# Optimization experiments

Measured on AMD Instinct MI355X. Metric: run time of the kernel, lower is better.

## Reference

```python
import jax, jax.numpy as jnp
import numpy as np

B, T, D = 4, 2048, 1024
E, K = 8, 2
H = int(D * 2.0)  # d_hidden


def setup_inputs() -> dict:
    key = jax.random.key(0)
    ks = jax.random.split(key, 7)
    x = jax.random.normal(ks[0], (B, T, D), dtype=jnp.float32)
    # router Linear(d_model, n_experts)
    router_w = jax.random.normal(ks[1], (D, E), dtype=jnp.float32) * (1.0 / np.sqrt(D))
    router_b = jnp.zeros((E,), dtype=jnp.float32)
    # expert weights, xavier_uniform-like scale
    lim1 = float(np.sqrt(6.0 / (D + H)))
    lim2 = float(np.sqrt(6.0 / (H + D)))
    w1 = jax.random.uniform(ks[2], (E, D, H), dtype=jnp.float32, minval=-lim1, maxval=lim1)
    b1 = jnp.zeros((E, H), dtype=jnp.float32)
    w2 = jax.random.uniform(ks[3], (E, H, D), dtype=jnp.float32, minval=-lim2, maxval=lim2)
    b2 = jnp.zeros((E, D), dtype=jnp.float32)
    return {"x": x, "router_w": router_w, "router_b": router_b,
            "w1": w1, "b1": b1, "w2": w2, "b2": b2}


def reference(x, router_w, router_b, w1, b1, w2, b2):
    Bs, Ts, d = x.shape
    N = Bs * Ts
    h = x.reshape(N, d)
    logits = h @ router_w + router_b                      # [N, E]
    probs = jax.nn.softmax(logits, axis=-1)
    weights, indices = jax.lax.top_k(probs, K)            # [N, K]
    weights = weights / (jnp.sum(weights, axis=-1, keepdims=True) + 1e-9)
    rows = jnp.arange(N)[:, None]
    # routing mask M and combine weights G (scatter over expert axis)
    M = jnp.zeros((N, E), dtype=bool).at[rows, indices].set(True)
    G = jnp.zeros((N, E), dtype=x.dtype).at[rows, indices].add(weights)
    # dense expert compute; tokens with G[:,e]==0 contribute nothing,
    # matching the masked gather/scatter loop exactly (dropout=0, eval mode)
    hidden = jax.nn.gelu(jnp.einsum('nd,edh->enh', h, w1) + b1[:, None, :],
                         approximate=False)               # [E, N, H]
    expert_out = jnp.einsum('enh,ehd->end', hidden, w2) + b2[:, None, :]  # [E, N, D]
    y = jnp.einsum('ne,end->nd', G, expert_out)           # combine
    y = y.reshape(Bs, Ts, d)
    # aux losses
    f_e = M.astype(jnp.float32).mean(axis=0)
    P_e = probs.mean(axis=0)
    lb_loss = -E * jnp.sum(f_e * P_e)
    z = jax.nn.logsumexp(logits, axis=-1)
    z_loss = jnp.mean(z ** 2)
    entropy = jnp.mean(-jnp.sum(probs * jnp.log(probs + 1e-10), axis=-1))
    return (y, lb_loss, z_loss, entropy, f_e, P_e)
```

## Files before the change

kernel.cpp:

```cpp
#include <hip/hip_runtime.h>
#include <hip/hip_bf16.h>

#define NTOK 8192
#define DM 1024
#define NE 8
#define DH 2048
#define CAP 18432

typedef __attribute__((ext_vector_type(8))) short short8;
typedef __attribute__((ext_vector_type(4))) float float4v;

#define ASYNC_COPY16(gsrc, ldst)                                                              \
    __builtin_amdgcn_global_load_lds((const __attribute__((address_space(1))) unsigned int*)(gsrc), \
                                     (__attribute__((address_space(3))) unsigned int*)(ldst), \
                                     16, 0, 0)

static __device__ __forceinline__ unsigned short f2bf(float f) {
    __hip_bfloat16 h = __float2bfloat16(f);
    return *reinterpret_cast<unsigned short*>(&h);
}

static __device__ __forceinline__ float fast_gelu(float v) {
    float x = v * 0.70710678118654752f;
    float ax = fabsf(x);
    float t = __frcp_rn(1.0f + 0.3275911f * ax);
    float poly = ((((1.061405429f * t - 1.453152027f) * t + 1.421413741f) * t
                   - 0.284496736f) * t + 0.254829592f) * t;
    float y = 1.0f - poly * __expf(-ax * ax);
    float erfv = copysignf(y, x);
    return 0.5f * v * (1.0f + erfv);
}


__global__ __launch_bounds__(256) void k_transpose(const float* __restrict__ src,
                                                   __hip_bfloat16* __restrict__ dst,
                                                   int R, int C) {
    __shared__ float t[64][65];
    size_t mat = (size_t)blockIdx.z * R * C;
    src += mat;
    dst += mat;
    int c0 = blockIdx.x * 64, r0 = blockIdx.y * 64;
    int tx = threadIdx.x & 63, ty = threadIdx.x >> 6;
#pragma unroll
    for (int i = 0; i < 16; i++) {
        int r = ty + i * 4;
        t[r][tx] = src[(size_t)(r0 + r) * C + c0 + tx];
    }
    __syncthreads();
    int rx = (threadIdx.x & 15) * 4;
    int cy = threadIdx.x >> 4;
#pragma unroll
    for (int i = 0; i < 4; i++) {
        int c = cy + i * 16;
        ushort4 v;
        v.x = f2bf(t[rx + 0][c]);
        v.y = f2bf(t[rx + 1][c]);
        v.z = f2bf(t[rx + 2][c]);
        v.w = f2bf(t[rx + 3][c]);
        *(ushort4*)((unsigned short*)dst + (size_t)(c0 + c) * R + r0 + rx) = v;
    }
}


__global__ __launch_bounds__(256) void k_router(const float* __restrict__ x,
                                                const float* __restrict__ rw,
                                                const float* __restrict__ rb,
                                                __hip_bfloat16* __restrict__ xb,
                                                int* __restrict__ topidx,
                                                float* __restrict__ topw,
                                                float* __restrict__ probs8,
                                                float* __restrict__ zent) {
    int lane = threadIdx.x & 63, wv = threadIdx.x >> 6;
    int n = blockIdx.x * 4 + wv;
    const float* xr = x + (size_t)n * DM;
    unsigned short* xbr = (unsigned short*)xb + (size_t)n * DM;
    float p[8] = {0.f, 0.f, 0.f, 0.f, 0.f, 0.f, 0.f, 0.f};
#pragma unroll
    for (int i = 0; i < 16; i++) {
        int d = lane + i * 64;
        float xv = xr[d];
        xbr[d] = f2bf(xv);
        const float4* w4 = (const float4*)(rw + (size_t)d * 8);
        float4 wa = w4[0], wb = w4[1];
        p[0] += xv * wa.x; p[1] += xv * wa.y; p[2] += xv * wa.z; p[3] += xv * wa.w;
        p[4] += xv * wb.x; p[5] += xv * wb.y; p[6] += xv * wb.z; p[7] += xv * wb.w;
    }
#pragma unroll
    for (int e = 0; e < 8; e++) {
#pragma unroll
        for (int off = 32; off > 0; off >>= 1) p[e] += __shfl_down(p[e], off);
    }
    if (lane == 0) {
        float logits[8], probs[8];
        float mx = -1e30f;
#pragma unroll
        for (int e = 0; e < 8; e++) {
            logits[e] = p[e] + rb[e];
            mx = fmaxf(mx, logits[e]);
        }
        float se = 0.f;
#pragma unroll
        for (int e = 0; e < 8; e++) {
            probs[e] = __expf(logits[e] - mx);
            se += probs[e];
        }
        float inv = 1.f / se;
        float z = mx + logf(se);
        float ent = 0.f;
#pragma unroll
        for (int e = 0; e < 8; e++) {
            probs[e] *= inv;
            ent -= probs[e] * logf(probs[e] + 1e-10f);
        }
        int i0 = 0;
#pragma unroll
        for (int e = 1; e < 8; e++)
            if (probs[e] > probs[i0]) i0 = e;
        int i1 = (i0 == 0) ? 1 : 0;
#pragma unroll
        for (int e = 0; e < 8; e++)
            if (e != i0 && e != i1 && probs[e] > probs[i1]) i1 = e;
        float w0 = probs[i0], w1v = probs[i1];
        float s = w0 + w1v + 1e-9f;
        topidx[2 * n] = i0;
        topidx[2 * n + 1] = i1;
        topw[2 * n] = w0 / s;
        topw[2 * n + 1] = w1v / s;
        float* pr = probs8 + (size_t)n * 8;
#pragma unroll
        for (int e = 0; e < 8; e++) pr[e] = probs[e];
        zent[2 * n] = z * z;
        zent[2 * n + 1] = ent;
    }
}


__global__ __launch_bounds__(256) void k_stats(const int* __restrict__ topidx,
                                               const float* __restrict__ probs8,
                                               const float* __restrict__ zent,
                                               float* __restrict__ fcnt,
                                               float* __restrict__ sump,
                                               float* __restrict__ szent) {
    int n = blockIdx.x * 256 + threadIdx.x;
    float v[18];
    int e0 = topidx[2 * n], e1 = topidx[2 * n + 1];
#pragma unroll
    for (int e = 0; e < 8; e++) v[e] = (float)((e == e0) + (e == e1));
    const float4* p4 = (const float4*)(probs8 + (size_t)n * 8);
    float4 pa = p4[0], pb = p4[1];
    v[8] = pa.x; v[9] = pa.y; v[10] = pa.z; v[11] = pa.w;
    v[12] = pb.x; v[13] = pb.y; v[14] = pb.z; v[15] = pb.w;
    v[16] = zent[2 * n];
    v[17] = zent[2 * n + 1];
#pragma unroll
    for (int i = 0; i < 18; i++)
#pragma unroll
        for (int off = 32; off > 0; off >>= 1) v[i] += __shfl_down(v[i], off);
    __shared__ float part[4][18];
    int lane = threadIdx.x & 63, wv = threadIdx.x >> 6;
    if (lane == 0)
#pragma unroll
        for (int i = 0; i < 18; i++) part[wv][i] = v[i];
    __syncthreads();
    if (threadIdx.x == 0) {
#pragma unroll
        for (int i = 0; i < 18; i++) {
            float s = part[0][i] + part[1][i] + part[2][i] + part[3][i];
            if (i < 8) atomicAdd(&fcnt[i], s);
            else if (i < 16) atomicAdd(&sump[i - 8], s);
            else atomicAdd(&szent[i - 16], s);
        }
    }
}


__global__ void k_scan(const float* __restrict__ fcnt, int* __restrict__ offs) {
    if (threadIdx.x == 0 && blockIdx.x == 0) {
        int o = 0;
        for (int e = 0; e < NE; e++) {
            offs[e] = o;
            int c = (int)(fcnt[e] + 0.5f);
            o += (c + 255) & ~255;
        }
        offs[NE] = o;
    }
}

__global__ __launch_bounds__(256) void k_scatter(const int* __restrict__ topidx,
                                                 const float* __restrict__ topw,
                                                 const int* __restrict__ offs,
                                                 int* __restrict__ cnt2,
                                                 int* __restrict__ rowtok,
                                                 float* __restrict__ roww) {
    __shared__ int lcnt[8], lbase[8];
    int tid = threadIdx.x;
    if (tid < 8) lcnt[tid] = 0;
    __syncthreads();
    int n = blockIdx.x * 256 + tid;
    int e0 = topidx[2 * n], e1 = topidx[2 * n + 1];
    int p0 = atomicAdd(&lcnt[e0], 1);
    int p1 = atomicAdd(&lcnt[e1], 1);
    __syncthreads();
    if (tid < 8) lbase[tid] = atomicAdd(&cnt2[tid], lcnt[tid]);
    __syncthreads();
    int r0 = offs[e0] + lbase[e0] + p0;
    int r1 = offs[e1] + lbase[e1] + p1;
    rowtok[r0] = n; roww[r0] = topw[2 * n];
    rowtok[r1] = n; roww[r1] = topw[2 * n + 1];
}


#define KT1 (DM / 32)

__global__ __launch_bounds__(512) void k_gemm1(const __hip_bfloat16* __restrict__ xb,
                                               const __hip_bfloat16* __restrict__ w1T,
                                               const float* __restrict__ b1,
                                               const int* __restrict__ rowtok,
                                               const int* __restrict__ offs,
                                               __hip_bfloat16* __restrict__ hid) {
    int bid = blockIdx.x;
    int ib = bid >> 3;
    int row0 = ((bid & 7) * 9 + (ib >> 4)) * 256;
    if (row0 >= offs[NE]) return;
    int h0 = (ib & 15) * 128;
    int e = 0;
    while (row0 >= offs[e + 1]) e++;
    int tid = threadIdx.x;

    __shared__ __align__(16) short lds[3][12288];
    __shared__ int tokoff[256];
    if (tid < 256) {
        int t = rowtok[row0 + tid];
        tokoff[tid] = (t < 0 ? 0 : t) * DM;
    }
    __syncthreads();

    int sr = tid >> 2, pc = tid & 3;
    int ch = pc ^ ((sr >> 1) & 3);
    const short* aS0 = (const short*)xb + tokoff[sr] + ch * 8;
    const short* aS1 = (const short*)xb + tokoff[128 + sr] + ch * 8;
    const short* bS  = (const short*)w1T + ((size_t)e * DH + h0 + sr) * DM + ch * 8;
    int ldo = sr * 32 + pc * 8;

    int lane = tid & 63, wv = tid >> 6;
    int wm = (wv >> 1) * 64, wn = (wv & 1) * 64;
    int quad = lane >> 4, l16 = lane & 15;
    int a_off[4], b_off[4];
#pragma unroll
    for (int mt = 0; mt < 4; mt++) {
        int r = wm + mt * 16 + l16;
        a_off[mt] = r * 32 + ((quad ^ ((r >> 1) & 3)) * 8);
    }
#pragma unroll
    for (int nt = 0; nt < 4; nt++) {
        int r = wn + nt * 16 + l16;
        b_off[nt] = 8192 + r * 32 + ((quad ^ ((r >> 1) & 3)) * 8);
    }
    float4v acc[4][4];
#pragma unroll
    for (int i = 0; i < 4; i++)
#pragma unroll
        for (int j = 0; j < 4; j++) {
            float4v z = {0.f, 0.f, 0.f, 0.f};
            acc[i][j] = z;
        }

    ASYNC_COPY16(aS0, &lds[0][ldo]);
    ASYNC_COPY16(aS1, &lds[0][4096 + ldo]);
    ASYNC_COPY16(bS,  &lds[0][8192 + ldo]);
    ASYNC_COPY16(aS0 + 32, &lds[1][ldo]);
    ASYNC_COPY16(aS1 + 32, &lds[1][4096 + ldo]);
    ASYNC_COPY16(bS + 32,  &lds[1][8192 + ldo]);
    asm volatile("s_waitcnt vmcnt(3)" ::: "memory");
    asm volatile("s_barrier" ::: "memory");

    int bi = 0;
#pragma unroll 1
    for (int t = 0; t < KT1; ++t) {
        const short* Ab = &lds[bi][0];
        int sbi = bi + 2; if (sbi >= 3) sbi -= 3;
        int k2 = (t + 2) * 32;
        short8 af[4], bf[4];
#pragma unroll
        for (int mt = 0; mt < 4; mt++) af[mt] = *(const short8*)(Ab + a_off[mt]);
#pragma unroll
        for (int nt = 0; nt < 4; nt++) bf[nt] = *(const short8*)(Ab + b_off[nt]);
        if (t + 2 < KT1) {
            ASYNC_COPY16(aS0 + k2, &lds[sbi][ldo]);
            ASYNC_COPY16(aS1 + k2, &lds[sbi][4096 + ldo]);
            ASYNC_COPY16(bS + k2,  &lds[sbi][8192 + ldo]);
        }
        __builtin_amdgcn_s_setprio(1);
#pragma unroll
        for (int mt = 0; mt < 4; mt++)
#pragma unroll
            for (int nt = 0; nt < 4; nt++)
                acc[mt][nt] = __builtin_amdgcn_mfma_f32_16x16x32_bf16(af[mt], bf[nt], acc[mt][nt], 0, 0, 0);
        __builtin_amdgcn_s_setprio(0);
        if (t + 2 < KT1) asm volatile("s_waitcnt vmcnt(3)" ::: "memory");
        else             asm volatile("s_waitcnt vmcnt(0)" ::: "memory");
        asm volatile("s_barrier" ::: "memory");
        bi++; if (bi == 3) bi = 0;
    }

    const float* b1e = b1 + (size_t)e * DH + h0;
#pragma unroll
    for (int mt = 0; mt < 4; mt++) {
#pragma unroll
        for (int nt = 0; nt < 4; nt++) {
            int rl = wm + mt * 16 + quad * 4;
            int cl = wn + nt * 16 + l16;
            float bias = b1e[cl];
#pragma unroll
            for (int r = 0; r < 4; r++) {
                float v = fast_gelu(acc[mt][nt][r] + bias);
                hid[(size_t)(row0 + rl + r) * DH + h0 + cl] = __float2bfloat16(v);
            }
        }
    }
}


#define KT2 (DH / 32)

__global__ __launch_bounds__(512) void k_gemm2(const __hip_bfloat16* __restrict__ hid,
                                               const __hip_bfloat16* __restrict__ w2T,
                                               const float* __restrict__ b2,
                                               const float* __restrict__ roww,
                                               const int* __restrict__ rowtok,
                                               const int* __restrict__ offs,
                                               float* __restrict__ y) {
    int bid = blockIdx.x;
    int ib = bid >> 3;
    int row0 = ((bid & 7) * 9 + (ib >> 3)) * 256;
    if (row0 >= offs[NE]) return;
    int d0 = (ib & 7) * 128;
    int e = 0;
    while (row0 >= offs[e + 1]) e++;
    int tid = threadIdx.x;

    __shared__ __align__(16) short lds[3][12288];
    __shared__ int tok_s[256];
    __shared__ float rw_s[256];
    if (tid < 256) {
        tok_s[tid] = rowtok[row0 + tid];
        rw_s[tid] = roww[row0 + tid];
    }
    __syncthreads();

    int sr = tid >> 2, pc = tid & 3;
    int ch = pc ^ ((sr >> 1) & 3);
    const short* aS0 = (const short*)hid + (size_t)(row0 + sr) * DH + ch * 8;
    const short* aS1 = (const short*)hid + (size_t)(row0 + 128 + sr) * DH + ch * 8;
    const short* bS  = (const short*)w2T + ((size_t)e * DM + d0 + sr) * DH + ch * 8;
    int ldo = sr * 32 + pc * 8;

    int lane = tid & 63, wv = tid >> 6;
    int wm = (wv >> 1) * 64, wn = (wv & 1) * 64;
    int quad = lane >> 4, l16 = lane & 15;
    int a_off[4], b_off[4];
#pragma unroll
    for (int mt = 0; mt < 4; mt++) {
        int r = wm + mt * 16 + l16;
        a_off[mt] = r * 32 + ((quad ^ ((r >> 1) & 3)) * 8);
    }
#pragma unroll
    for (int nt = 0; nt < 4; nt++) {
        int r = wn + nt * 16 + l16;
        b_off[nt] = 8192 + r * 32 + ((quad ^ ((r >> 1) & 3)) * 8);
    }
    float4v acc[4][4];
#pragma unroll
    for (int i = 0; i < 4; i++)
#pragma unroll
        for (int j = 0; j < 4; j++) {
            float4v z = {0.f, 0.f, 0.f, 0.f};
            acc[i][j] = z;
        }

    ASYNC_COPY16(aS0, &lds[0][ldo]);
    ASYNC_COPY16(aS1, &lds[0][4096 + ldo]);
    ASYNC_COPY16(bS,  &lds[0][8192 + ldo]);
    ASYNC_COPY16(aS0 + 32, &lds[1][ldo]);
    ASYNC_COPY16(aS1 + 32, &lds[1][4096 + ldo]);
    ASYNC_COPY16(bS + 32,  &lds[1][8192 + ldo]);
    asm volatile("s_waitcnt vmcnt(3)" ::: "memory");
    asm volatile("s_barrier" ::: "memory");

    int bi = 0;
#pragma unroll 1
    for (int t = 0; t < KT2; ++t) {
        const short* Ab = &lds[bi][0];
        int sbi = bi + 2; if (sbi >= 3) sbi -= 3;
        int k2 = (t + 2) * 32;
        short8 af[4], bf[4];
#pragma unroll
        for (int mt = 0; mt < 4; mt++) af[mt] = *(const short8*)(Ab + a_off[mt]);
#pragma unroll
        for (int nt = 0; nt < 4; nt++) bf[nt] = *(const short8*)(Ab + b_off[nt]);
        if (t + 2 < KT2) {
            ASYNC_COPY16(aS0 + k2, &lds[sbi][ldo]);
            ASYNC_COPY16(aS1 + k2, &lds[sbi][4096 + ldo]);
            ASYNC_COPY16(bS + k2,  &lds[sbi][8192 + ldo]);
        }
        __builtin_amdgcn_s_setprio(1);
#pragma unroll
        for (int mt = 0; mt < 4; mt++)
#pragma unroll
            for (int nt = 0; nt < 4; nt++)
                acc[mt][nt] = __builtin_amdgcn_mfma_f32_16x16x32_bf16(af[mt], bf[nt], acc[mt][nt], 0, 0, 0);
        __builtin_amdgcn_s_setprio(0);
        if (t + 2 < KT2) asm volatile("s_waitcnt vmcnt(3)" ::: "memory");
        else             asm volatile("s_waitcnt vmcnt(0)" ::: "memory");
        asm volatile("s_barrier" ::: "memory");
        bi++; if (bi == 3) bi = 0;
    }

    const float* b2e = b2 + (size_t)e * DM + d0;
#pragma unroll
    for (int mt = 0; mt < 4; mt++) {
#pragma unroll
        for (int nt = 0; nt < 4; nt++) {
            int rl = wm + mt * 16 + quad * 4;
            int cl = wn + nt * 16 + l16;
            float bias = b2e[cl];
#pragma unroll
            for (int r = 0; r < 4; r++) {
                int lr = rl + r;
                int tk = tok_s[lr];
                if (tk >= 0) {
                    float v = (acc[mt][nt][r] + bias) * rw_s[lr];
                    atomicAdd(&y[(size_t)tk * DM + d0 + cl], v);
                }
            }
        }
    }
}


__global__ void k_finalize(const float* __restrict__ fcnt, const float* __restrict__ sump,
                           const float* __restrict__ szent, float* __restrict__ out) {
    if (threadIdx.x == 0 && blockIdx.x == 0) {
        const float invN = 1.0f / (float)NTOK;
        float lb = 0.f;
        float f[NE], P[NE];
        for (int e = 0; e < NE; e++) {
            f[e] = fcnt[e] * invN;
            P[e] = sump[e] * invN;
            lb += f[e] * P[e];
        }
        size_t base = (size_t)NTOK * DM;
        out[base + 0] = -(float)NE * lb;
        out[base + 1] = szent[0] * invN;
        out[base + 2] = szent[1] * invN;
        for (int e = 0; e < NE; e++) out[base + 3 + e] = f[e];
        for (int e = 0; e < NE; e++) out[base + 11 + e] = P[e];
    }
}


extern "C" void kernel_launch(void* const* d_in, const int* in_sizes, int n_in,
                              void* d_out, int out_size, void* d_ws, size_t ws_size,
                              hipStream_t stream) {
    const float* x  = (const float*)d_in[0];
    const float* rw = (const float*)d_in[1];
    const float* rb = (const float*)d_in[2];
    const float* w1 = (const float*)d_in[3];
    const float* b1 = (const float*)d_in[4];
    const float* w2 = (const float*)d_in[5];
    const float* b2 = (const float*)d_in[6];
    float* out = (float*)d_out;

    char* ws = (char*)d_ws;
    size_t o = 0;
    auto alloc = [&](size_t bytes) {
        size_t r = o;
        o = (o + bytes + 255) & ~(size_t)255;
        return r;
    };
    __hip_bfloat16* w1T = (__hip_bfloat16*)(ws + alloc((size_t)NE * DM * DH * 2));
    __hip_bfloat16* w2T = (__hip_bfloat16*)(ws + alloc((size_t)NE * DM * DH * 2));
    __hip_bfloat16* xb  = (__hip_bfloat16*)(ws + alloc((size_t)NTOK * DM * 2));
    __hip_bfloat16* hid = (__hip_bfloat16*)(ws + alloc((size_t)CAP * DH * 2));
    int* rowtok = (int*)(ws + alloc(CAP * 4));
    size_t zstart = o;
    float* roww  = (float*)(ws + alloc(CAP * 4));
    float* fcnt  = (float*)(ws + alloc(64));
    int* cnt2    = (int*)(ws + alloc(64));
    int* offs    = (int*)(ws + alloc(64));
    float* sump  = (float*)(ws + alloc(64));
    float* szent = (float*)(ws + alloc(64));
    size_t zend = o;
    int* topidx = (int*)(ws + alloc((size_t)NTOK * 2 * 4));
    float* topw = (float*)(ws + alloc((size_t)NTOK * 2 * 4));
    float* probs8 = (float*)(ws + alloc((size_t)NTOK * 8 * 4));
    float* zent   = (float*)(ws + alloc((size_t)NTOK * 2 * 4));

    hipMemsetAsync(rowtok, 0xFF, (size_t)CAP * 4, stream);
    hipMemsetAsync(ws + zstart, 0, zend - zstart, stream);
    hipMemsetAsync(out, 0, (size_t)NTOK * DM * 4, stream);

    k_transpose<<<dim3(DH / 64, DM / 64, NE), 256, 0, stream>>>(w1, w1T, DM, DH);
    k_transpose<<<dim3(DM / 64, DH / 64, NE), 256, 0, stream>>>(w2, w2T, DH, DM);
    k_router<<<NTOK / 4, 256, 0, stream>>>(x, rw, rb, xb, topidx, topw, probs8, zent);
    k_stats<<<NTOK / 256, 256, 0, stream>>>(topidx, probs8, zent, fcnt, sump, szent);
    k_scan<<<1, 1, 0, stream>>>(fcnt, offs);
    k_scatter<<<NTOK / 256, 256, 0, stream>>>(topidx, topw, offs, cnt2, rowtok, roww);
    k_gemm1<<<1152, 512, 0, stream>>>(xb, w1T, b1, rowtok, offs, hid);
    k_gemm2<<<576, 512, 0, stream>>>(hid, w2T, b2, roww, rowtok, offs, out);
    k_finalize<<<1, 1, 0, stream>>>(fcnt, sump, szent, out);
}
```

Measured before the change: 496.1 us.

## Replace atomic scatter-add with per-slot output buffer and combine kernel; double-buffer GEMMs

GEMM2 now writes each expert row's weighted output to a dense per-slot buffer, and a new combine kernel sums each token's two slots into y. This removes the fp32 atomicAdd scatter and the memset of the output. Both GEMMs also drop from three to two LDS stages, which frees shared memory so the launch bound can target more resident blocks. The cost is an extra 75MB buffer written and read back, plus a shallower prefetch pipeline that waits on every load each iteration.

Result: slower. 1.670 ms (+236.6%).

```diff
diff --git a/kernel.cpp b/kernel.cpp
--- a/kernel.cpp
+++ b/kernel.cpp
@@ -191,7 +191,8 @@
                                                  const int* __restrict__ offs,
                                                  int* __restrict__ cnt2,
                                                  int* __restrict__ rowtok,
-                                                 float* __restrict__ roww) {
+                                                 float* __restrict__ roww,
+                                                 int* __restrict__ slot) {
     __shared__ int lcnt[8], lbase[8];
     int tid = threadIdx.x;
     if (tid < 8) lcnt[tid] = 0;
@@ -205,19 +206,19 @@
     __syncthreads();
     int r0 = offs[e0] + lbase[e0] + p0;
     int r1 = offs[e1] + lbase[e1] + p1;
-    rowtok[r0] = n; roww[r0] = topw[2 * n];
-    rowtok[r1] = n; roww[r1] = topw[2 * n + 1];
+    rowtok[r0] = n; roww[r0] = topw[2 * n];     slot[2 * n] = r0;
+    rowtok[r1] = n; roww[r1] = topw[2 * n + 1]; slot[2 * n + 1] = r1;
 }
 
 
 #define KT1 (DM / 32)
 
-__global__ __launch_bounds__(512) void k_gemm1(const __hip_bfloat16* __restrict__ xb,
-                                               const __hip_bfloat16* __restrict__ w1T,
-                                               const float* __restrict__ b1,
-                                               const int* __restrict__ rowtok,
-                                               const int* __restrict__ offs,
-                                               __hip_bfloat16* __restrict__ hid) {
+__global__ __launch_bounds__(512, 6) void k_gemm1(const __hip_bfloat16* __restrict__ xb,
+                                                  const __hip_bfloat16* __restrict__ w1T,
+                                                  const float* __restrict__ b1,
+                                                  const int* __restrict__ rowtok,
+                                                  const int* __restrict__ offs,
+                                                  __hip_bfloat16* __restrict__ hid) {
     int bid = blockIdx.x;
     int ib = bid >> 3;
     int row0 = ((bid & 7) * 9 + (ib >> 4)) * 256;
@@ -227,7 +228,7 @@
     while (row0 >= offs[e + 1]) e++;
     int tid = threadIdx.x;
 
-    __shared__ __align__(16) short lds[3][12288];
+    __shared__ __align__(16) short lds[2][12288];
     __shared__ int tokoff[256];
     if (tid < 256) {
         int t = rowtok[row0 + tid];
@@ -268,28 +269,24 @@
     ASYNC_COPY16(aS0, &lds[0][ldo]);
     ASYNC_COPY16(aS1, &lds[0][4096 + ldo]);
     ASYNC_COPY16(bS,  &lds[0][8192 + ldo]);
-    ASYNC_COPY16(aS0 + 32, &lds[1][ldo]);
-    ASYNC_COPY16(aS1 + 32, &lds[1][4096 + ldo]);
-    ASYNC_COPY16(bS + 32,  &lds[1][8192 + ldo]);
-    asm volatile("s_waitcnt vmcnt(3)" ::: "memory");
+    asm volatile("s_waitcnt vmcnt(0)" ::: "memory");
     asm volatile("s_barrier" ::: "memory");
 
-    int bi = 0;
+    int buf = 0;
 #pragma unroll 1
     for (int t = 0; t < KT1; ++t) {
-        const short* Ab = &lds[bi][0];
-        int sbi = bi + 2; if (sbi >= 3) sbi -= 3;
-        int k2 = (t + 2) * 32;
+        const short* Ab = &lds[buf][0];
+        int k1 = (t + 1) * 32;
+        if (t + 1 < KT1) {
+            ASYNC_COPY16(aS0 + k1, &lds[buf ^ 1][ldo]);
+            ASYNC_COPY16(aS1 + k1, &lds[buf ^ 1][4096 + ldo]);
+            ASYNC_COPY16(bS + k1,  &lds[buf ^ 1][8192 + ldo]);
+        }
         short8 af[4], bf[4];
 #pragma unroll
         for (int mt = 0; mt < 4; mt++) af[mt] = *(const short8*)(Ab + a_off[mt]);
 #pragma unroll
         for (int nt = 0; nt < 4; nt++) bf[nt] = *(const short8*)(Ab + b_off[nt]);
-        if (t + 2 < KT1) {
-            ASYNC_COPY16(aS0 + k2, &lds[sbi][ldo]);
-            ASYNC_COPY16(aS1 + k2, &lds[sbi][4096 + ldo]);
-            ASYNC_COPY16(bS + k2,  &lds[sbi][8192 + ldo]);
-        }
         __builtin_amdgcn_s_setprio(1);
 #pragma unroll
         for (int mt = 0; mt < 4; mt++)
@@ -297,10 +294,9 @@
             for (int nt = 0; nt < 4; nt++)
                 acc[mt][nt] = __builtin_amdgcn_mfma_f32_16x16x32_bf16(af[mt], bf[nt], acc[mt][nt], 0, 0, 0);
         __builtin_amdgcn_s_setprio(0);
-        if (t + 2 < KT1) asm volatile("s_waitcnt vmcnt(3)" ::: "memory");
-        else             asm volatile("s_waitcnt vmcnt(0)" ::: "memory");
+        asm volatile("s_waitcnt vmcnt(0)" ::: "memory");
         asm volatile("s_barrier" ::: "memory");
-        bi++; if (bi == 3) bi = 0;
+        buf ^= 1;
     }
 
     const float* b1e = b1 + (size_t)e * DH + h0;
@@ -323,13 +319,12 @@
 
 #define KT2 (DH / 32)
 
-__global__ __launch_bounds__(512) void k_gemm2(const __hip_bfloat16* __restrict__ hid,
-                                               const __hip_bfloat16* __restrict__ w2T,
-                                               const float* __restrict__ b2,
-                                               const float* __restrict__ roww,
-                                               const int* __restrict__ rowtok,
-                                               const int* __restrict__ offs,
-                                               float* __restrict__ y) {
+__global__ __launch_bounds__(512, 6) void k_gemm2(const __hip_bfloat16* __restrict__ hid,
+                                                  const __hip_bfloat16* __restrict__ w2T,
+                                                  const float* __restrict__ b2,
+                                                  const float* __restrict__ roww,
+                                                  const int* __restrict__ offs,
+                                                  float* __restrict__ outb) {
     int bid = blockIdx.x;
     int ib = bid >> 3;
     int row0 = ((bid & 7) * 9 + (ib >> 3)) * 256;
@@ -339,14 +334,7 @@
     while (row0 >= offs[e + 1]) e++;
     int tid = threadIdx.x;
 
-    __shared__ __align__(16) short lds[3][12288];
-    __shared__ int tok_s[256];
-    __shared__ float rw_s[256];
-    if (tid < 256) {
-        tok_s[tid] = rowtok[row0 + tid];
-        rw_s[tid] = roww[row0 + tid];
-    }
-    __syncthreads();
+    __shared__ __align__(16) short lds[2][12288];
 
     int sr = tid >> 2, pc = tid & 3;
     int ch = pc ^ ((sr >> 1) & 3);
@@ -381,28 +369,24 @@
     ASYNC_COPY16(aS0, &lds[0][ldo]);
     ASYNC_COPY16(aS1, &lds[0][4096 + ldo]);
     ASYNC_COPY16(bS,  &lds[0][8192 + ldo]);
-    ASYNC_COPY16(aS0 + 32, &lds[1][ldo]);
-    ASYNC_COPY16(aS1 + 32, &lds[1][4096 + ldo]);
-    ASYNC_COPY16(bS + 32,  &lds[1][8192 + ldo]);
-    asm volatile("s_waitcnt vmcnt(3)" ::: "memory");
+    asm volatile("s_waitcnt vmcnt(0)" ::: "memory");
     asm volatile("s_barrier" ::: "memory");
 
-    int bi = 0;
+    int buf = 0;
 #pragma unroll 1
     for (int t = 0; t < KT2; ++t) {
-        const short* Ab = &lds[bi][0];
-        int sbi = bi + 2; if (sbi >= 3) sbi -= 3;
-        int k2 = (t + 2) * 32;
+        const short* Ab = &lds[buf][0];
+        int k1 = (t + 1) * 32;
+        if (t + 1 < KT2) {
+            ASYNC_COPY16(aS0 + k1, &lds[buf ^ 1][ldo]);
+            ASYNC_COPY16(aS1 + k1, &lds[buf ^ 1][4096 + ldo]);
+            ASYNC_COPY16(bS + k1,  &lds[buf ^ 1][8192 + ldo]);
+        }
         short8 af[4], bf[4];
 #pragma unroll
         for (int mt = 0; mt < 4; mt++) af[mt] = *(const short8*)(Ab + a_off[mt]);
 #pragma unroll
         for (int nt = 0; nt < 4; nt++) bf[nt] = *(const short8*)(Ab + b_off[nt]);
-        if (t + 2 < KT2) {
-            ASYNC_COPY16(aS0 + k2, &lds[sbi][ldo]);
-            ASYNC_COPY16(aS1 + k2, &lds[sbi][4096 + ldo]);
-            ASYNC_COPY16(bS + k2,  &lds[sbi][8192 + ldo]);
-        }
         __builtin_amdgcn_s_setprio(1);
 #pragma unroll
         for (int mt = 0; mt < 4; mt++)
@@ -410,10 +394,9 @@
             for (int nt = 0; nt < 4; nt++)
                 acc[mt][nt] = __builtin_amdgcn_mfma_f32_16x16x32_bf16(af[mt], bf[nt], acc[mt][nt], 0, 0, 0);
         __builtin_amdgcn_s_setprio(0);
-        if (t + 2 < KT2) asm volatile("s_waitcnt vmcnt(3)" ::: "memory");
-        else             asm volatile("s_waitcnt vmcnt(0)" ::: "memory");
+        asm volatile("s_waitcnt vmcnt(0)" ::: "memory");
         asm volatile("s_barrier" ::: "memory");
-        bi++; if (bi == 3) bi = 0;
+        buf ^= 1;
     }
 
     const float* b2e = b2 + (size_t)e * DM + d0;
@@ -426,17 +409,30 @@
             float bias = b2e[cl];
 #pragma unroll
             for (int r = 0; r < 4; r++) {
-                int lr = rl + r;
-                int tk = tok_s[lr];
-                if (tk >= 0) {
-                    float v = (acc[mt][nt][r] + bias) * rw_s[lr];
-                    atomicAdd(&y[(size_t)tk * DM + d0 + cl], v);
-                }
+                int grow = row0 + rl + r;
+                float v = (acc[mt][nt][r] + bias) * roww[grow];
+                outb[(size_t)grow * DM + d0 + cl] = v;
             }
         }
     }
 }
 
+
+__global__ __launch_bounds__(256) void k_combine(const float* __restrict__ outb,
+                                                 const int* __restrict__ slot,
+                                                 float* __restrict__ y) {
+    int n = blockIdx.x;
+    int r0 = slot[2 * n], r1 = slot[2 * n + 1];
+    const float4* p0 = (const float4*)(outb + (size_t)r0 * DM);
+    const float4* p1 = (const float4*)(outb + (size_t)r1 * DM);
+    float4 a = p0[threadIdx.x], b = p1[threadIdx.x];
+    float4 c;
+    c.x = a.x + b.x;
+    c.y = a.y + b.y;
+    c.z = a.z + b.z;
+    c.w = a.w + b.w;
+    ((float4*)(y + (size_t)n * DM))[threadIdx.x] = c;
+}
 
 __global__ void k_finalize(const float* __restrict__ fcnt, const float* __restrict__ sump,
                            const float* __restrict__ szent, float* __restrict__ out) {
@@ -482,6 +478,7 @@
     __hip_bfloat16* w2T = (__hip_bfloat16*)(ws + alloc((size_t)NE * DM * DH * 2));
     __hip_bfloat16* xb  = (__hip_bfloat16*)(ws + alloc((size_t)NTOK * DM * 2));
     __hip_bfloat16* hid = (__hip_bfloat16*)(ws + alloc((size_t)CAP * DH * 2));
+    float* outb = (float*)(ws + alloc((size_t)CAP * DM * 4));
     int* rowtok = (int*)(ws + alloc(CAP * 4));
     size_t zstart = o;
     float* roww  = (float*)(ws + alloc(CAP * 4));
@@ -493,20 +490,21 @@
     size_t zend = o;
     int* topidx = (int*)(ws + alloc((size_t)NTOK * 2 * 4));
     float* topw = (float*)(ws + alloc((size_t)NTOK * 2 * 4));
+    int* slot   = (int*)(ws + alloc((size_t)NTOK * 2 * 4));
     float* probs8 = (float*)(ws + alloc((size_t)NTOK * 8 * 4));
     float* zent   = (float*)(ws + alloc((size_t)NTOK * 2 * 4));
 
     hipMemsetAsync(rowtok, 0xFF, (size_t)CAP * 4, stream);
     hipMemsetAsync(ws + zstart, 0, zend - zstart, stream);
-    hipMemsetAsync(out, 0, (size_t)NTOK * DM * 4, stream);
 
     k_transpose<<<dim3(DH / 64, DM / 64, NE), 256, 0, stream>>>(w1, w1T, DM, DH);
     k_transpose<<<dim3(DM / 64, DH / 64, NE), 256, 0, stream>>>(w2, w2T, DH, DM);
     k_router<<<NTOK / 4, 256, 0, stream>>>(x, rw, rb, xb, topidx, topw, probs8, zent);
     k_stats<<<NTOK / 256, 256, 0, stream>>>(topidx, probs8, zent, fcnt, sump, szent);
     k_scan<<<1, 1, 0, stream>>>(fcnt, offs);
-    k_scatter<<<NTOK / 256, 256, 0, stream>>>(topidx, topw, offs, cnt2, rowtok, roww);
+    k_scatter<<<NTOK / 256, 256, 0, stream>>>(topidx, topw, offs, cnt2, rowtok, roww, slot);
     k_gemm1<<<1152, 512, 0, stream>>>(xb, w1T, b1, rowtok, offs, hid);
-    k_gemm2<<<576, 512, 0, stream>>>(hid, w2T, b2, roww, rowtok, offs, out);
+    k_gemm2<<<576, 512, 0, stream>>>(hid, w2T, b2, roww, offs, outb);
+    k_combine<<<NTOK, 256, 0, stream>>>(outb, slot, out);
     k_finalize<<<1, 1, 0, stream>>>(fcnt, sump, szent, out);
 }
```

## Fuse routing stats/scan/scatter into one kernel; replace atomic combine with gather pass

Applied to the files above, without the earlier changes.

Replaces the stats, scan, scatter and finalize kernels plus three memsets with a single-block routing kernel. It uses wave ballots to assign rows deterministically and computes the aux losses in the same pass. GEMM2 now writes weighted per-row outputs to a buffer instead of doing atomicAdd into y, and a new combine kernel sums each token's two rows. It also adds an extra barrier and sched_barriers in both GEMM main loops. The cost is an extra 75MB fp32 buffer round trip, and the single-block routing kernel is serial over 8192 tokens.

After: 536.5 us. +8.1%, slower.

```diff
diff --git a/kernel.cpp b/kernel.cpp
--- a/kernel.cpp
+++ b/kernel.cpp
@@ -135,78 +135,94 @@
 }
 
 
-__global__ __launch_bounds__(256) void k_stats(const int* __restrict__ topidx,
-                                               const float* __restrict__ probs8,
-                                               const float* __restrict__ zent,
-                                               float* __restrict__ fcnt,
-                                               float* __restrict__ sump,
-                                               float* __restrict__ szent) {
-    int n = blockIdx.x * 256 + threadIdx.x;
-    float v[18];
-    int e0 = topidx[2 * n], e1 = topidx[2 * n + 1];
-#pragma unroll
-    for (int e = 0; e < 8; e++) v[e] = (float)((e == e0) + (e == e1));
-    const float4* p4 = (const float4*)(probs8 + (size_t)n * 8);
-    float4 pa = p4[0], pb = p4[1];
-    v[8] = pa.x; v[9] = pa.y; v[10] = pa.z; v[11] = pa.w;
-    v[12] = pb.x; v[13] = pb.y; v[14] = pb.z; v[15] = pb.w;
-    v[16] = zent[2 * n];
-    v[17] = zent[2 * n + 1];
-#pragma unroll
-    for (int i = 0; i < 18; i++)
-#pragma unroll
-        for (int off = 32; off > 0; off >>= 1) v[i] += __shfl_down(v[i], off);
-    __shared__ float part[4][18];
-    int lane = threadIdx.x & 63, wv = threadIdx.x >> 6;
+__global__ __launch_bounds__(512) void k_route_aux(const int* __restrict__ topidx,
+                                                   const float* __restrict__ topw,
+                                                   const float* __restrict__ probs8,
+                                                   const float* __restrict__ zent,
+                                                   int* __restrict__ rowtok,
+                                                   float* __restrict__ roww,
+                                                   int* __restrict__ slot,
+                                                   int* __restrict__ offs,
+                                                   float* __restrict__ out) {
+    int tid = threadIdx.x, lane = tid & 63, wv = tid >> 6;
+    __shared__ int cnt_s[8];
+    __shared__ int offs_s[9];
+    __shared__ float red[8][10];
+    unsigned long long ltmask = ((unsigned long long)1 << lane) - 1ull;
+
+    int cnt = 0;
+    for (int i = lane; i < NTOK; i += 64) {
+        int2 v = ((const int2*)topidx)[i];
+        unsigned long long m0 = __ballot(v.x == wv);
+        unsigned long long m1 = __ballot(v.y == wv);
+        cnt += __popcll(m0) + __popcll(m1);
+    }
+    if (lane == 0) cnt_s[wv] = cnt;
+    __syncthreads();
+    if (tid == 0) {
+        int o = 0;
+        for (int e = 0; e < NE; e++) { offs_s[e] = o; o += (cnt_s[e] + 255) & ~255; }
+        offs_s[NE] = o;
+        for (int e = 0; e <= NE; e++) offs[e] = offs_s[e];
+    }
+    __syncthreads();
+    int base = offs_s[wv], pos = 0;
+    for (int i = lane; i < NTOK; i += 64) {
+        int2 v = ((const int2*)topidx)[i];
+        float2 w = ((const float2*)topw)[i];
+        unsigned long long m0 = __ballot(v.x == wv);
+        if (v.x == wv) {
+            int r = base + pos + __popcll(m0 & ltmask);
+            rowtok[r] = i; roww[r] = w.x; slot[2 * i] = r;
+        }
+        pos += __popcll(m0);
+        unsigned long long m1 = __ballot(v.y == wv);
+        if (v.y == wv) {
+            int r = base + pos + __popcll(m1 & ltmask);
+            rowtok[r] = i; roww[r] = w.y; slot[2 * i + 1] = r;
+        }
+        pos += __popcll(m1);
+    }
+    for (int r = base + cnt + lane; r < offs_s[wv + 1]; r += 64) {
+        rowtok[r] = -1; roww[r] = 0.f;
+    }
+    float s[10];
+#pragma unroll
+    for (int k = 0; k < 10; k++) s[k] = 0.f;
+    for (int i = tid; i < NTOK; i += 512) {
+        const float4* p4 = (const float4*)(probs8 + (size_t)i * 8);
+        float4 pa = p4[0], pb = p4[1];
+        s[0] += pa.x; s[1] += pa.y; s[2] += pa.z; s[3] += pa.w;
+        s[4] += pb.x; s[5] += pb.y; s[6] += pb.z; s[7] += pb.w;
+        float2 ze = ((const float2*)zent)[i];
+        s[8] += ze.x; s[9] += ze.y;
+    }
+#pragma unroll
+    for (int k = 0; k < 10; k++)
+#pragma unroll
+        for (int off = 32; off > 0; off >>= 1) s[k] += __shfl_down(s[k], off);
     if (lane == 0)
 #pragma unroll
-        for (int i = 0; i < 18; i++) part[wv][i] = v[i];
+        for (int k = 0; k < 10; k++) red[wv][k] = s[k];
     __syncthreads();
-    if (threadIdx.x == 0) {
-#pragma unroll
-        for (int i = 0; i < 18; i++) {
-            float s = part[0][i] + part[1][i] + part[2][i] + part[3][i];
-            if (i < 8) atomicAdd(&fcnt[i], s);
-            else if (i < 16) atomicAdd(&sump[i - 8], s);
-            else atomicAdd(&szent[i - 16], s);
-        }
-    }
-}
-
-
-__global__ void k_scan(const float* __restrict__ fcnt, int* __restrict__ offs) {
-    if (threadIdx.x == 0 && blockIdx.x == 0) {
-        int o = 0;
+    if (tid == 0) {
+        const float invN = 1.0f / (float)NTOK;
+        float lb = 0.f;
+        size_t b = (size_t)NTOK * DM;
         for (int e = 0; e < NE; e++) {
-            offs[e] = o;
-            int c = (int)(fcnt[e] + 0.5f);
-            o += (c + 255) & ~255;
-        }
-        offs[NE] = o;
-    }
-}
-
-__global__ __launch_bounds__(256) void k_scatter(const int* __restrict__ topidx,
-                                                 const float* __restrict__ topw,
-                                                 const int* __restrict__ offs,
-                                                 int* __restrict__ cnt2,
-                                                 int* __restrict__ rowtok,
-                                                 float* __restrict__ roww) {
-    __shared__ int lcnt[8], lbase[8];
-    int tid = threadIdx.x;
-    if (tid < 8) lcnt[tid] = 0;
-    __syncthreads();
-    int n = blockIdx.x * 256 + tid;
-    int e0 = topidx[2 * n], e1 = topidx[2 * n + 1];
-    int p0 = atomicAdd(&lcnt[e0], 1);
-    int p1 = atomicAdd(&lcnt[e1], 1);
-    __syncthreads();
-    if (tid < 8) lbase[tid] = atomicAdd(&cnt2[tid], lcnt[tid]);
-    __syncthreads();
-    int r0 = offs[e0] + lbase[e0] + p0;
-    int r1 = offs[e1] + lbase[e1] + p1;
-    rowtok[r0] = n; roww[r0] = topw[2 * n];
-    rowtok[r1] = n; roww[r1] = topw[2 * n + 1];
+            float sP = 0.f;
+            for (int w8 = 0; w8 < 8; w8++) sP += red[w8][e];
+            float fe = cnt_s[e] * invN, Pe = sP * invN;
+            lb += fe * Pe;
+            out[b + 3 + e] = fe;
+            out[b + 11 + e] = Pe;
+        }
+        float z2 = 0.f, en = 0.f;
+        for (int w8 = 0; w8 < 8; w8++) { z2 += red[w8][8]; en += red[w8][9]; }
+        out[b + 0] = -(float)NE * lb;
+        out[b + 1] = z2 * invN;
+        out[b + 2] = en * invN;
+    }
 }
 
 
@@ -290,6 +306,8 @@
             ASYNC_COPY16(aS1 + k2, &lds[sbi][4096 + ldo]);
             ASYNC_COPY16(bS + k2,  &lds[sbi][8192 + ldo]);
         }
+        asm volatile("s_barrier" ::: "memory");
+        __builtin_amdgcn_sched_barrier(0);
         __builtin_amdgcn_s_setprio(1);
 #pragma unroll
         for (int mt = 0; mt < 4; mt++)
@@ -297,6 +315,7 @@
             for (int nt = 0; nt < 4; nt++)
                 acc[mt][nt] = __builtin_amdgcn_mfma_f32_16x16x32_bf16(af[mt], bf[nt], acc[mt][nt], 0, 0, 0);
         __builtin_amdgcn_s_setprio(0);
+        __builtin_amdgcn_sched_barrier(0);
         if (t + 2 < KT1) asm volatile("s_waitcnt vmcnt(3)" ::: "memory");
         else             asm volatile("s_waitcnt vmcnt(0)" ::: "memory");
         asm volatile("s_barrier" ::: "memory");
@@ -327,9 +346,8 @@
                                                const __hip_bfloat16* __restrict__ w2T,
                                                const float* __restrict__ b2,
                                                const float* __restrict__ roww,
-                                               const int* __restrict__ rowtok,
                                                const int* __restrict__ offs,
-                                               float* __restrict__ y) {
+                                               float* __restrict__ outb) {
     int bid = blockIdx.x;
     int ib = bid >> 3;
     int row0 = ((bid & 7) * 9 + (ib >> 3)) * 256;
@@ -340,13 +358,6 @@
     int tid = threadIdx.x;
 
     __shared__ __align__(16) short lds[3][12288];
-    __shared__ int tok_s[256];
-    __shared__ float rw_s[256];
-    if (tid < 256) {
-        tok_s[tid] = rowtok[row0 + tid];
-        rw_s[tid] = roww[row0 + tid];
-    }
-    __syncthreads();
 
     int sr = tid >> 2, pc = tid & 3;
     int ch = pc ^ ((sr >> 1) & 3);
@@ -403,6 +414,8 @@
             ASYNC_COPY16(aS1 + k2, &lds[sbi][4096 + ldo]);
             ASYNC_COPY16(bS + k2,  &lds[sbi][8192 + ldo]);
         }
+        asm volatile("s_barrier" ::: "memory");
+        __builtin_amdgcn_sched_barrier(0);
         __builtin_amdgcn_s_setprio(1);
 #pragma unroll
         for (int mt = 0; mt < 4; mt++)
@@ -410,6 +423,7 @@
             for (int nt = 0; nt < 4; nt++)
                 acc[mt][nt] = __builtin_amdgcn_mfma_f32_16x16x32_bf16(af[mt], bf[nt], acc[mt][nt], 0, 0, 0);
         __builtin_amdgcn_s_setprio(0);
+        __builtin_amdgcn_sched_barrier(0);
         if (t + 2 < KT2) asm volatile("s_waitcnt vmcnt(3)" ::: "memory");
         else             asm volatile("s_waitcnt vmcnt(0)" ::: "memory");
         asm volatile("s_barrier" ::: "memory");
@@ -426,36 +440,29 @@
             float bias = b2e[cl];
 #pragma unroll
             for (int r = 0; r < 4; r++) {
-                int lr = rl + r;
-                int tk = tok_s[lr];
-                if (tk >= 0) {
-                    float v = (acc[mt][nt][r] + bias) * rw_s[lr];
-                    atomicAdd(&y[(size_t)tk * DM + d0 + cl], v);
-                }
+                int grow = row0 + rl + r;
+                float v = (acc[mt][nt][r] + bias) * roww[grow];
+                outb[(size_t)grow * DM + d0 + cl] = v;
             }
         }
     }
 }
 
 
-__global__ void k_finalize(const float* __restrict__ fcnt, const float* __restrict__ sump,
-                           const float* __restrict__ szent, float* __restrict__ out) {
-    if (threadIdx.x == 0 && blockIdx.x == 0) {
-        const float invN = 1.0f / (float)NTOK;
-        float lb = 0.f;
-        float f[NE], P[NE];
-        for (int e = 0; e < NE; e++) {
-            f[e] = fcnt[e] * invN;
-            P[e] = sump[e] * invN;
-            lb += f[e] * P[e];
-        }
-        size_t base = (size_t)NTOK * DM;
-        out[base + 0] = -(float)NE * lb;
-        out[base + 1] = szent[0] * invN;
-        out[base + 2] = szent[1] * invN;
-        for (int e = 0; e < NE; e++) out[base + 3 + e] = f[e];
-        for (int e = 0; e < NE; e++) out[base + 11 + e] = P[e];
-    }
+__global__ __launch_bounds__(256) void k_combine(const float* __restrict__ outb,
+                                                 const int* __restrict__ slot,
+                                                 float* __restrict__ y) {
+    int n = blockIdx.x;
+    int r0 = slot[2 * n], r1 = slot[2 * n + 1];
+    const float4* p0 = (const float4*)(outb + (size_t)r0 * DM);
+    const float4* p1 = (const float4*)(outb + (size_t)r1 * DM);
+    float4 a = p0[threadIdx.x], b = p1[threadIdx.x];
+    float4 c;
+    c.x = a.x + b.x;
+    c.y = a.y + b.y;
+    c.z = a.z + b.z;
+    c.w = a.w + b.w;
+    ((float4*)(y + (size_t)n * DM))[threadIdx.x] = c;
 }
 
 
@@ -482,31 +489,21 @@
     __hip_bfloat16* w2T = (__hip_bfloat16*)(ws + alloc((size_t)NE * DM * DH * 2));
     __hip_bfloat16* xb  = (__hip_bfloat16*)(ws + alloc((size_t)NTOK * DM * 2));
     __hip_bfloat16* hid = (__hip_bfloat16*)(ws + alloc((size_t)CAP * DH * 2));
+    float* outb = (float*)(ws + alloc((size_t)CAP * DM * 4));
     int* rowtok = (int*)(ws + alloc(CAP * 4));
-    size_t zstart = o;
-    float* roww  = (float*)(ws + alloc(CAP * 4));
-    float* fcnt  = (float*)(ws + alloc(64));
-    int* cnt2    = (int*)(ws + alloc(64));
-    int* offs    = (int*)(ws + alloc(64));
-    float* sump  = (float*)(ws + alloc(64));
-    float* szent = (float*)(ws + alloc(64));
-    size_t zend = o;
+    float* roww = (float*)(ws + alloc(CAP * 4));
+    int* offs   = (int*)(ws + alloc(64));
     int* topidx = (int*)(ws + alloc((size_t)NTOK * 2 * 4));
     float* topw = (float*)(ws + alloc((size_t)NTOK * 2 * 4));
+    int* slot   = (int*)(ws + alloc((size_t)NTOK * 2 * 4));
     float* probs8 = (float*)(ws + alloc((size_t)NTOK * 8 * 4));
     float* zent   = (float*)(ws + alloc((size_t)NTOK * 2 * 4));
-
-    hipMemsetAsync(rowtok, 0xFF, (size_t)CAP * 4, stream);
-    hipMemsetAsync(ws + zstart, 0, zend - zstart, stream);
-    hipMemsetAsync(out, 0, (size_t)NTOK * DM * 4, stream);
 
     k_transpose<<<dim3(DH / 64, DM / 64, NE), 256, 0, stream>>>(w1, w1T, DM, DH);
     k_transpose<<<dim3(DM / 64, DH / 64, NE), 256, 0, stream>>>(w2, w2T, DH, DM);
     k_router<<<NTOK / 4, 256, 0, stream>>>(x, rw, rb, xb, topidx, topw, probs8, zent);
-    k_stats<<<NTOK / 256, 256, 0, stream>>>(topidx, probs8, zent, fcnt, sump, szent);
-    k_scan<<<1, 1, 0, stream>>>(fcnt, offs);
-    k_scatter<<<NTOK / 256, 256, 0, stream>>>(topidx, topw, offs, cnt2, rowtok, roww);
+    k_route_aux<<<1, 512, 0, stream>>>(topidx, topw, probs8, zent, rowtok, roww, slot, offs, out);
     k_gemm1<<<1152, 512, 0, stream>>>(xb, w1T, b1, rowtok, offs, hid);
-    k_gemm2<<<576, 512, 0, stream>>>(hid, w2T, b2, roww, rowtok, offs, out);
-    k_finalize<<<1, 1, 0, stream>>>(fcnt, sump, szent, out);
-}
+    k_gemm2<<<576, 512, 0, stream>>>(hid, w2T, b2, roww, offs, outb);
+    k_combine<<<NTOK, 256, 0, stream>>>(outb, slot, out);
+}
```
